# Kernel optimization log

Hardware: AMD Instinct MI355X
Metric: run time of the kernel (lower is better)

The kernel has to match this reference:

```python
import math
import jax, jax.numpy as jnp
import numpy as np

S = 4096          # total packed tokens (b*s with bsz=1)
NUM_HEADS = 16
HEAD_DIM = 80
SCALE = 1.0 / math.sqrt(HEAD_DIM)


def setup_inputs() -> dict:
    key = jax.random.key(0)
    kq, kk, kv = jax.random.split(key, 3)
    q = jax.random.normal(kq, (S, NUM_HEADS, HEAD_DIM), dtype=jnp.float32)
    k = jax.random.normal(kk, (S, NUM_HEADS, HEAD_DIM), dtype=jnp.float32)
    v = jax.random.normal(kv, (S, NUM_HEADS, HEAD_DIM), dtype=jnp.float32)
    # 4 packed sequences of 1024 tokens each (flatten_batch=True, bsz=1)
    cu_seqlens = jnp.array([0, 1024, 2048, 3072, 4096], dtype=jnp.int32)
    return {"q": q, "k": k, "v": v, "bsz": 1, "cu_seqlens": cu_seqlens}


def reference(q, k, v, bsz, cu_seqlens):
    # q/k/v: [(b s), h, d]; flatten_batch=True so bsz == 1
    s = q.shape[0] // bsz
    h, d = q.shape[1], q.shape[2]

    # Block-diagonal mask from cu_seqlens: True inside each packed sequence.
    seg = jnp.searchsorted(cu_seqlens[1:], jnp.arange(s), side="right")  # [s]
    mask = seg[:, None] == seg[None, :]                                  # [s, s]

    # '(b s) h d -> b h s d'
    qb = q.reshape(bsz, s, h, d).transpose(0, 2, 1, 3)
    kb = k.reshape(bsz, s, h, d).transpose(0, 2, 1, 3)
    vb = v.reshape(bsz, s, h, d).transpose(0, 2, 1, 3)

    scores = jnp.einsum("bhsd,bhtd->bhst", qb, kb) * SCALE
    bias = jnp.where(mask, jnp.zeros((), scores.dtype), jnp.finfo(scores.dtype).min)
    attn = jax.nn.softmax((scores + bias).astype(jnp.float32), axis=-1).astype(q.dtype)

    out = jnp.einsum("bhst,bhtd->bhsd", attn, vb)
    # 'b h s d -> (b s) h d'
    return out.transpose(0, 2, 1, 3).reshape(bsz * s, h, d)
```

## Files before the change

kernel.cpp:

```cpp
#include <hip/hip_runtime.h>
#include <hip/hip_bf16.h>
#include <math.h>

#define NTOK 4096
#define NH 16
#define HD 80
#define TOKSTRIDE (NH * HD)
#define QBLK 64
#define KVBLK 64
#define KSTR 88
#define VSTR 72
#define KLBYTES (65 * KSTR * 2)

typedef __bf16 bf16x4 __attribute__((ext_vector_type(4)));
typedef __bf16 bf16x8 __attribute__((ext_vector_type(8)));
typedef float  f32x4  __attribute__((ext_vector_type(4)));
typedef short  short4v __attribute__((ext_vector_type(4)));

#if __has_builtin(__builtin_amdgcn_mfma_f32_16x16x16bf16_1k)
__device__ inline f32x4 mfma16(bf16x4 a, bf16x4 b, f32x4 c) {
  return __builtin_amdgcn_mfma_f32_16x16x16bf16_1k(
      __builtin_bit_cast(short4v, a), __builtin_bit_cast(short4v, b), c, 0, 0, 0);
}
#elif __has_builtin(__builtin_amdgcn_mfma_f32_16x16x16_bf16)
__device__ inline f32x4 mfma16(bf16x4 a, bf16x4 b, f32x4 c) {
  return __builtin_amdgcn_mfma_f32_16x16x16_bf16(a, b, c, 0, 0, 0);
}
#else
__device__ inline f32x4 mfma16(bf16x4 a, bf16x4 b, f32x4 c) {
  asm volatile("v_mfma_f32_16x16x16_bf16 %0, %1, %2, %0"
               : "+v"(c) : "v"(a), "v"(b));
  return c;
}
#endif

__global__ __launch_bounds__(256)
void prepack(const float* __restrict__ kg, const float* __restrict__ vg,
             __bf16* __restrict__ kb, __bf16* __restrict__ vtb) {
  __shared__ __align__(16) __bf16 Vl[HD][72];
  const int tid  = threadIdx.x;
  const int tok0 = blockIdx.x * 64;
  const int h    = blockIdx.y;

  for (int i = tid; i < 64 * 20; i += 256) {
    const int row = i / 20;
    const int c4  = (i % 20) * 4;
    const size_t gsrc = (size_t)(tok0 + row) * TOKSTRIDE + h * HD + c4;
    const size_t gdst = ((size_t)h * NTOK + tok0 + row) * HD + c4;

    float4 fk = *reinterpret_cast<const float4*>(kg + gsrc);
    bf16x4 uk;
    uk[0] = (__bf16)fk.x; uk[1] = (__bf16)fk.y;
    uk[2] = (__bf16)fk.z; uk[3] = (__bf16)fk.w;
    *reinterpret_cast<bf16x4*>(kb + gdst) = uk;

    float4 fv = *reinterpret_cast<const float4*>(vg + gsrc);
    Vl[c4 + 0][row] = (__bf16)fv.x; Vl[c4 + 1][row] = (__bf16)fv.y;
    Vl[c4 + 2][row] = (__bf16)fv.z; Vl[c4 + 3][row] = (__bf16)fv.w;
  }
  __syncthreads();
  for (int i = tid; i < HD * 16; i += 256) {
    const int d = i / 16;
    const int b = i % 16;
    const int pb = ((b & 3) << 2) | (b >> 2);
    bf16x4 val = *reinterpret_cast<const bf16x4*>(&Vl[d][b * 4]);
    *reinterpret_cast<bf16x4*>(vtb + ((size_t)h * HD + d) * NTOK + tok0 + pb * 4) = val;
  }
}

__global__ __launch_bounds__(256, 4)
void vis_attn13(const float* __restrict__ qg, const __bf16* __restrict__ kb,
                const __bf16* __restrict__ vtb, const int* __restrict__ cu,
                int n_cu, float* __restrict__ outg) {
  __shared__ __align__(16) unsigned char smem[22960];
  __bf16* Kl = reinterpret_cast<__bf16*>(smem);
  __bf16* Vt = reinterpret_cast<__bf16*>(smem + KLBYTES);

  const int tid  = threadIdx.x;
  const int w    = tid >> 6;
  const int lane = tid & 63;
  const int lr   = lane & 15;
  const int g    = lane >> 4;

  const int q0 = blockIdx.x * QBLK;
  const int h  = blockIdx.y;

  int kv_start = 0, kv_end = NTOK;
  for (int i = 0; i + 1 < n_cu; ++i) {
    int a = cu[i], b = cu[i + 1];
    if (q0 >= a && q0 < b) { kv_start = a; kv_end = b; }
  }

  for (int i = tid; i < 512 + KSTR; i += 256) {
    if (i < 512) Kl[(i >> 3) * KSTR + 80 + (i & 7)] = (__bf16)0.0f;
    else         Kl[64 * KSTR + (i - 512)]          = (__bf16)0.0f;
  }

  const float qscale = 1.4426950408889634f / sqrtf((float)HD);
  const int qrow = q0 + w * 16 + lr;
  const float* qrp = qg + (size_t)qrow * TOKSTRIDE + h * HD;
  bf16x8 qf[3];
  #pragma unroll
  for (int c = 0; c < 3; ++c) {
    const int dbase = c * 32 + g * 8;
    if (dbase < HD) {
      float4 f0 = *reinterpret_cast<const float4*>(qrp + dbase);
      float4 f1 = *reinterpret_cast<const float4*>(qrp + dbase + 4);
      qf[c][0] = (__bf16)(f0.x * qscale); qf[c][1] = (__bf16)(f0.y * qscale);
      qf[c][2] = (__bf16)(f0.z * qscale); qf[c][3] = (__bf16)(f0.w * qscale);
      qf[c][4] = (__bf16)(f1.x * qscale); qf[c][5] = (__bf16)(f1.y * qscale);
      qf[c][6] = (__bf16)(f1.z * qscale); qf[c][7] = (__bf16)(f1.w * qscale);
    } else {
      #pragma unroll
      for (int j = 0; j < 8; ++j) qf[c][j] = (__bf16)0.0f;
    }
  }

  bf16x4 vfl;
  #pragma unroll
  for (int j = 0; j < 4; ++j) vfl[j] = (lr == 0) ? (__bf16)1.0f : (__bf16)0.0f;

  f32x4 O[6];
  #pragma unroll
  for (int n = 0; n < 6; ++n) O[n] = (f32x4){0.f, 0.f, 0.f, 0.f};

  const __bf16* kbh  = kb  + (size_t)h * NTOK * HD;
  const __bf16* vtbh = vtb + (size_t)h * HD * NTOK;
  const char* gbase = reinterpret_cast<const char*>(kbh);
  const int vdelta = (int)(reinterpret_cast<const char*>(vtbh) - gbase);

  int goff[5], ginc[5], ldsoff[5];
  #pragma unroll
  for (int j = 0; j < 5; ++j) {
    const int c = tid + j * 256;
    if (c < 640) {
      const int row = c / 10, col = (c % 10) * 8;
      goff[j]   = (kv_start * HD + row * HD + col) * 2;
      ginc[j]   = KVBLK * HD * 2;
      ldsoff[j] = (row * KSTR + col) * 2;
    } else {
      const int c2 = c - 640, d = c2 / 8, kc = (c2 % 8) * 8;
      goff[j]   = vdelta + (kv_start + d * NTOK + kc) * 2;
      ginc[j]   = KVBLK * 2;
      ldsoff[j] = KLBYTES + (d * VSTR + kc) * 2;
    }
  }

  bf16x8 st[5];
  #pragma unroll
  for (int j = 0; j < 5; ++j) {
    st[j] = *reinterpret_cast<const bf16x8*>(gbase + goff[j]);
    goff[j] += ginc[j];
  }

  for (int kv0 = kv_start; kv0 < kv_end; kv0 += KVBLK) {
    __syncthreads();
    #pragma unroll
    for (int j = 0; j < 5; ++j)
      *reinterpret_cast<bf16x8*>(smem + ldsoff[j]) = st[j];
    __syncthreads();

    if (kv0 + KVBLK < kv_end) {
      #pragma unroll
      for (int j = 0; j < 5; ++j) {
        st[j] = *reinterpret_cast<const bf16x8*>(gbase + goff[j]);
        goff[j] += ginc[j];
      }
    }

    bf16x4 pf[4];
    __builtin_amdgcn_s_setprio(1);
    #pragma unroll
    for (int t = 0; t < 4; ++t) {
      f32x4 S = (f32x4){0.f, 0.f, 0.f, 0.f};
      #pragma unroll
      for (int c = 0; c < 3; ++c) {
        bf16x8 kf = *reinterpret_cast<const bf16x8*>(&Kl[(t * 16 + lr) * KSTR + c * 32 + g * 8]);
        S = __builtin_amdgcn_mfma_f32_16x16x32_bf16(kf, qf[c], S, 0, 0, 0);
      }
      #pragma unroll
      for (int r = 0; r < 4; ++r)
        pf[t][r] = (__bf16)exp2f(S[r]);
    }
    __builtin_amdgcn_s_setprio(0);

    __builtin_amdgcn_s_setprio(1);
    #pragma unroll
    for (int n = 0; n < 5; ++n) {
      bf16x8 v01 = *reinterpret_cast<const bf16x8*>(&Vt[(n * 16 + lr) * VSTR + g * 16]);
      bf16x8 v23 = *reinterpret_cast<const bf16x8*>(&Vt[(n * 16 + lr) * VSTR + g * 16 + 8]);
      bf16x4 vf0 = __builtin_shufflevector(v01, v01, 0, 1, 2, 3);
      bf16x4 vf1 = __builtin_shufflevector(v01, v01, 4, 5, 6, 7);
      bf16x4 vf2 = __builtin_shufflevector(v23, v23, 0, 1, 2, 3);
      bf16x4 vf3 = __builtin_shufflevector(v23, v23, 4, 5, 6, 7);
      O[n] = mfma16(pf[0], vf0, O[n]);
      O[n] = mfma16(pf[1], vf1, O[n]);
      O[n] = mfma16(pf[2], vf2, O[n]);
      O[n] = mfma16(pf[3], vf3, O[n]);
    }
    #pragma unroll
    for (int t = 0; t < 4; ++t)
      O[5] = mfma16(pf[t], vfl, O[5]);
    __builtin_amdgcn_s_setprio(0);
  }

  float inv[4];
  #pragma unroll
  for (int r = 0; r < 4; ++r) {
    float l = __shfl(O[5][r], lane & 48);
    inv[r] = 1.0f / l;
  }
  const int orow0 = q0 + w * 16 + g * 4;
  #pragma unroll
  for (int n = 0; n < 5; ++n) {
    #pragma unroll
    for (int r = 0; r < 4; ++r)
      outg[(size_t)(orow0 + r) * TOKSTRIDE + h * HD + n * 16 + lr] = O[n][r] * inv[r];
  }
}

__global__ __launch_bounds__(256, 4)
void vis_attn_fb(const float* __restrict__ qg, const float* __restrict__ kg,
                 const float* __restrict__ vg, const int* __restrict__ cu,
                 int n_cu, float* __restrict__ outg) {
  __shared__ __align__(16) __bf16 Kl[KVBLK][104];
  __shared__ __align__(16) __bf16 Vt[HD][72];
  __shared__ __align__(16) __bf16 Pl[64][72];

  const int tid  = threadIdx.x;
  const int w    = tid >> 6;
  const int lane = tid & 63;
  const int lr   = lane & 15;
  const int g    = lane >> 4;
  const int q0 = blockIdx.x * 64;
  const int h  = blockIdx.y;

  int kv_start = 0, kv_end = NTOK;
  for (int i = 0; i + 1 < n_cu; ++i) {
    int a = cu[i], b = cu[i + 1];
    if (q0 >= a && q0 < b) { kv_start = a; kv_end = b; }
  }
  for (int i = tid; i < KVBLK * 16; i += 256)
    Kl[i >> 4][HD + (i & 15)] = (__bf16)0.0f;

  const float qscale = 1.4426950408889634f / sqrtf((float)HD);
  const int qrow = q0 + w * 16 + lr;
  const float* qptr = qg + (size_t)qrow * TOKSTRIDE + h * HD;
  bf16x8 qf[3];
  #pragma unroll
  for (int c = 0; c < 3; ++c) {
    const int dbase = c * 32 + g * 8;
    if (dbase < HD) {
      float4 f0 = *reinterpret_cast<const float4*>(qptr + dbase);
      float4 f1 = *reinterpret_cast<const float4*>(qptr + dbase + 4);
      qf[c][0] = (__bf16)(f0.x * qscale); qf[c][1] = (__bf16)(f0.y * qscale);
      qf[c][2] = (__bf16)(f0.z * qscale); qf[c][3] = (__bf16)(f0.w * qscale);
      qf[c][4] = (__bf16)(f1.x * qscale); qf[c][5] = (__bf16)(f1.y * qscale);
      qf[c][6] = (__bf16)(f1.z * qscale); qf[c][7] = (__bf16)(f1.w * qscale);
    } else {
      #pragma unroll
      for (int j = 0; j < 8; ++j) qf[c][j] = (__bf16)0.0f;
    }
  }

  f32x4 O[5];
  #pragma unroll
  for (int n = 0; n < 5; ++n) O[n] = (f32x4){0.f, 0.f, 0.f, 0.f};
  float m_run[4] = {-1e30f, -1e30f, -1e30f, -1e30f};
  float l_run[4] = {0.f, 0.f, 0.f, 0.f};

  for (int kv0 = kv_start; kv0 < kv_end; kv0 += KVBLK) {
    __syncthreads();
    for (int i = tid; i < KVBLK * (HD / 4); i += 256) {
      const int row = i / (HD / 4);
      const int c4  = (i % (HD / 4)) * 4;
      float4 f = *reinterpret_cast<const float4*>(
          kg + (size_t)(kv0 + row) * TOKSTRIDE + h * HD + c4);
      Kl[row][c4 + 0] = (__bf16)f.x; Kl[row][c4 + 1] = (__bf16)f.y;
      Kl[row][c4 + 2] = (__bf16)f.z; Kl[row][c4 + 3] = (__bf16)f.w;
    }
    for (int i = tid; i < KVBLK * (HD / 4); i += 256) {
      const int row = i / (HD / 4);
      const int c4  = (i % (HD / 4)) * 4;
      float4 f = *reinterpret_cast<const float4*>(
          vg + (size_t)(kv0 + row) * TOKSTRIDE + h * HD + c4);
      Vt[c4 + 0][row] = (__bf16)f.x; Vt[c4 + 1][row] = (__bf16)f.y;
      Vt[c4 + 2][row] = (__bf16)f.z; Vt[c4 + 3][row] = (__bf16)f.w;
    }
    __syncthreads();

    f32x4 S[4];
    #pragma unroll
    for (int t = 0; t < 4; ++t) {
      S[t] = (f32x4){0.f, 0.f, 0.f, 0.f};
      #pragma unroll
      for (int c = 0; c < 3; ++c) {
        bf16x8 kf = *reinterpret_cast<const bf16x8*>(&Kl[t * 16 + lr][c * 32 + g * 8]);
        S[t] = __builtin_amdgcn_mfma_f32_16x16x32_bf16(qf[c], kf, S[t], 0, 0, 0);
      }
    }
    float pmax[4];
    #pragma unroll
    for (int r = 0; r < 4; ++r)
      pmax[r] = fmaxf(fmaxf(S[0][r], S[1][r]), fmaxf(S[2][r], S[3][r]));
    #pragma unroll
    for (int r = 0; r < 4; ++r) {
      pmax[r] = fmaxf(pmax[r], __shfl_xor(pmax[r], 1));
      pmax[r] = fmaxf(pmax[r], __shfl_xor(pmax[r], 2));
      pmax[r] = fmaxf(pmax[r], __shfl_xor(pmax[r], 4));
      pmax[r] = fmaxf(pmax[r], __shfl_xor(pmax[r], 8));
    }
    float alpha[4];
    #pragma unroll
    for (int r = 0; r < 4; ++r) {
      float mn = fmaxf(m_run[r], pmax[r]);
      alpha[r] = exp2f(m_run[r] - mn);
      m_run[r] = mn;
    }
    #pragma unroll
    for (int t = 0; t < 4; ++t) {
      #pragma unroll
      for (int r = 0; r < 4; ++r)
        S[t][r] = exp2f(S[t][r] - m_run[r]);
    }
    float rsum[4];
    #pragma unroll
    for (int r = 0; r < 4; ++r) {
      rsum[r] = (S[0][r] + S[1][r]) + (S[2][r] + S[3][r]);
      rsum[r] += __shfl_xor(rsum[r], 1);
      rsum[r] += __shfl_xor(rsum[r], 2);
      rsum[r] += __shfl_xor(rsum[r], 4);
      rsum[r] += __shfl_xor(rsum[r], 8);
      l_run[r] = l_run[r] * alpha[r] + rsum[r];
    }
    #pragma unroll
    for (int n = 0; n < 5; ++n) {
      #pragma unroll
      for (int r = 0; r < 4; ++r) O[n][r] *= alpha[r];
    }
    #pragma unroll
    for (int t = 0; t < 4; ++t) {
      #pragma unroll
      for (int r = 0; r < 4; ++r)
        Pl[w * 16 + g * 4 + r][t * 16 + lr] = (__bf16)S[t][r];
    }
    #pragma unroll
    for (int kc = 0; kc < 2; ++kc) {
      bf16x8 pf = *reinterpret_cast<const bf16x8*>(&Pl[w * 16 + lr][kc * 32 + g * 8]);
      #pragma unroll
      for (int n = 0; n < 5; ++n) {
        bf16x8 vf = *reinterpret_cast<const bf16x8*>(&Vt[n * 16 + lr][kc * 32 + g * 8]);
        O[n] = __builtin_amdgcn_mfma_f32_16x16x32_bf16(pf, vf, O[n], 0, 0, 0);
      }
    }
  }

  float inv[4];
  #pragma unroll
  for (int r = 0; r < 4; ++r) inv[r] = 1.0f / l_run[r];
  const int orow0 = q0 + w * 16 + g * 4;
  #pragma unroll
  for (int n = 0; n < 5; ++n) {
    #pragma unroll
    for (int r = 0; r < 4; ++r)
      outg[(size_t)(orow0 + r) * TOKSTRIDE + h * HD + n * 16 + lr] = O[n][r] * inv[r];
  }
}

extern "C" void kernel_launch(void* const* d_in, const int* in_sizes, int n_in,
                              void* d_out, int out_size, void* d_ws, size_t ws_size,
                              hipStream_t stream) {
  const float* q  = (const float*)d_in[0];
  const float* k  = (const float*)d_in[1];
  const float* v  = (const float*)d_in[2];
  const int* cu   = (const int*)d_in[4];
  const int n_cu  = in_sizes[4];
  float* out      = (float*)d_out;

  const size_t one = (size_t)NH * NTOK * HD * sizeof(__bf16);

  if (ws_size >= 2 * one) {
    __bf16* kbuf = (__bf16*)d_ws;
    __bf16* vtb  = (__bf16*)((char*)d_ws + one);
    dim3 gp(NTOK / 64, NH);
    prepack<<<gp, 256, 0, stream>>>(k, v, kbuf, vtb);
    dim3 ga(NTOK / QBLK, NH);
    vis_attn13<<<ga, 256, 0, stream>>>(q, kbuf, vtb, cu, n_cu, out);
  } else {
    dim3 gf(NTOK / 64, NH);
    vis_attn_fb<<<gf, 256, 0, stream>>>(q, k, v, cu, n_cu, out);
  }
}
```

Measured before the change: 57.84 us.

## Interleave QK and PV per key tile and overlap head-dim chunk loads

The attention loop now computes exp scores for one 16-key tile and immediately feeds them into the PV MFMAs, instead of materialising all four tiles first. The V transpose in prepack drops its permuted layout for plain contiguous 8-element stores, and the kernel reads V fragments directly per tile. The third QK chunk now reads K columns 48..79 with a Q fragment zeroed for the low half, so the zero-padded K columns and the extra LDS row are no longer needed. This shrinks register pressure and LDS setup, at the cost of an overlapping redundant K read and a different MFMA dependency pattern.

```diff
diff --git a/kernel.cpp b/kernel.cpp
--- a/kernel.cpp
+++ b/kernel.cpp
@@ -10,7 +10,7 @@
 #define KVBLK 64
 #define KSTR 88
 #define VSTR 72
-#define KLBYTES (65 * KSTR * 2)
+#define KLBYTES (64 * KSTR * 2)
 
 typedef __bf16 bf16x4 __attribute__((ext_vector_type(4)));
 typedef __bf16 bf16x8 __attribute__((ext_vector_type(8)));
@@ -59,20 +59,19 @@
     Vl[c4 + 2][row] = (__bf16)fv.z; Vl[c4 + 3][row] = (__bf16)fv.w;
   }
   __syncthreads();
-  for (int i = tid; i < HD * 16; i += 256) {
-    const int d = i / 16;
-    const int b = i % 16;
-    const int pb = ((b & 3) << 2) | (b >> 2);
-    bf16x4 val = *reinterpret_cast<const bf16x4*>(&Vl[d][b * 4]);
-    *reinterpret_cast<bf16x4*>(vtb + ((size_t)h * HD + d) * NTOK + tok0 + pb * 4) = val;
+  for (int i = tid; i < HD * 8; i += 256) {
+    const int d  = i / 8;
+    const int c8 = (i % 8) * 8;
+    bf16x8 val = *reinterpret_cast<const bf16x8*>(&Vl[d][c8]);
+    *reinterpret_cast<bf16x8*>(vtb + ((size_t)h * HD + d) * NTOK + tok0 + c8) = val;
   }
 }
 
 __global__ __launch_bounds__(256, 4)
-void vis_attn13(const float* __restrict__ qg, const __bf16* __restrict__ kb,
+void vis_attn15(const float* __restrict__ qg, const __bf16* __restrict__ kb,
                 const __bf16* __restrict__ vtb, const int* __restrict__ cu,
                 int n_cu, float* __restrict__ outg) {
-  __shared__ __align__(16) unsigned char smem[22960];
+  __shared__ __align__(16) unsigned char smem[22784];
   __bf16* Kl = reinterpret_cast<__bf16*>(smem);
   __bf16* Vt = reinterpret_cast<__bf16*>(smem + KLBYTES);
 
@@ -91,29 +90,32 @@
     if (q0 >= a && q0 < b) { kv_start = a; kv_end = b; }
   }
 
-  for (int i = tid; i < 512 + KSTR; i += 256) {
-    if (i < 512) Kl[(i >> 3) * KSTR + 80 + (i & 7)] = (__bf16)0.0f;
-    else         Kl[64 * KSTR + (i - 512)]          = (__bf16)0.0f;
-  }
-
   const float qscale = 1.4426950408889634f / sqrtf((float)HD);
   const int qrow = q0 + w * 16 + lr;
   const float* qrp = qg + (size_t)qrow * TOKSTRIDE + h * HD;
-  bf16x8 qf[3];
-  #pragma unroll
-  for (int c = 0; c < 3; ++c) {
+  bf16x8 qf[2];
+  #pragma unroll
+  for (int c = 0; c < 2; ++c) {
     const int dbase = c * 32 + g * 8;
-    if (dbase < HD) {
-      float4 f0 = *reinterpret_cast<const float4*>(qrp + dbase);
-      float4 f1 = *reinterpret_cast<const float4*>(qrp + dbase + 4);
-      qf[c][0] = (__bf16)(f0.x * qscale); qf[c][1] = (__bf16)(f0.y * qscale);
-      qf[c][2] = (__bf16)(f0.z * qscale); qf[c][3] = (__bf16)(f0.w * qscale);
-      qf[c][4] = (__bf16)(f1.x * qscale); qf[c][5] = (__bf16)(f1.y * qscale);
-      qf[c][6] = (__bf16)(f1.z * qscale); qf[c][7] = (__bf16)(f1.w * qscale);
-    } else {
-      #pragma unroll
-      for (int j = 0; j < 8; ++j) qf[c][j] = (__bf16)0.0f;
-    }
+    float4 f0 = *reinterpret_cast<const float4*>(qrp + dbase);
+    float4 f1 = *reinterpret_cast<const float4*>(qrp + dbase + 4);
+    qf[c][0] = (__bf16)(f0.x * qscale); qf[c][1] = (__bf16)(f0.y * qscale);
+    qf[c][2] = (__bf16)(f0.z * qscale); qf[c][3] = (__bf16)(f0.w * qscale);
+    qf[c][4] = (__bf16)(f1.x * qscale); qf[c][5] = (__bf16)(f1.y * qscale);
+    qf[c][6] = (__bf16)(f1.z * qscale); qf[c][7] = (__bf16)(f1.w * qscale);
+  }
+  bf16x8 qf2;
+  if (g >= 2) {
+    const int dbase = 48 + g * 8;
+    float4 f0 = *reinterpret_cast<const float4*>(qrp + dbase);
+    float4 f1 = *reinterpret_cast<const float4*>(qrp + dbase + 4);
+    qf2[0] = (__bf16)(f0.x * qscale); qf2[1] = (__bf16)(f0.y * qscale);
+    qf2[2] = (__bf16)(f0.z * qscale); qf2[3] = (__bf16)(f0.w * qscale);
+    qf2[4] = (__bf16)(f1.x * qscale); qf2[5] = (__bf16)(f1.y * qscale);
+    qf2[6] = (__bf16)(f1.z * qscale); qf2[7] = (__bf16)(f1.w * qscale);
+  } else {
+    #pragma unroll
+    for (int j = 0; j < 8; ++j) qf2[j] = (__bf16)0.0f;
   }
 
   bf16x4 vfl;
@@ -168,39 +170,31 @@
       }
     }
 
-    bf16x4 pf[4];
     __builtin_amdgcn_s_setprio(1);
     #pragma unroll
     for (int t = 0; t < 4; ++t) {
+      const int krow = (t * 16 + lr) * KSTR;
       f32x4 S = (f32x4){0.f, 0.f, 0.f, 0.f};
-      #pragma unroll
-      for (int c = 0; c < 3; ++c) {
-        bf16x8 kf = *reinterpret_cast<const bf16x8*>(&Kl[(t * 16 + lr) * KSTR + c * 32 + g * 8]);
-        S = __builtin_amdgcn_mfma_f32_16x16x32_bf16(kf, qf[c], S, 0, 0, 0);
-      }
+      {
+        bf16x8 kf0 = *reinterpret_cast<const bf16x8*>(&Kl[krow + g * 8]);
+        bf16x8 kf1 = *reinterpret_cast<const bf16x8*>(&Kl[krow + 32 + g * 8]);
+        bf16x8 kf2 = *reinterpret_cast<const bf16x8*>(&Kl[krow + 48 + g * 8]);
+        S = __builtin_amdgcn_mfma_f32_16x16x32_bf16(kf0, qf[0], S, 0, 0, 0);
+        S = __builtin_amdgcn_mfma_f32_16x16x32_bf16(kf1, qf[1], S, 0, 0, 0);
+        S = __builtin_amdgcn_mfma_f32_16x16x32_bf16(kf2, qf2, S, 0, 0, 0);
+      }
+      bf16x4 pf;
       #pragma unroll
       for (int r = 0; r < 4; ++r)
-        pf[t][r] = (__bf16)exp2f(S[r]);
-    }
-    __builtin_amdgcn_s_setprio(0);
-
-    __builtin_amdgcn_s_setprio(1);
-    #pragma unroll
-    for (int n = 0; n < 5; ++n) {
-      bf16x8 v01 = *reinterpret_cast<const bf16x8*>(&Vt[(n * 16 + lr) * VSTR + g * 16]);
-      bf16x8 v23 = *reinterpret_cast<const bf16x8*>(&Vt[(n * 16 + lr) * VSTR + g * 16 + 8]);
-      bf16x4 vf0 = __builtin_shufflevector(v01, v01, 0, 1, 2, 3);
-      bf16x4 vf1 = __builtin_shufflevector(v01, v01, 4, 5, 6, 7);
-      bf16x4 vf2 = __builtin_shufflevector(v23, v23, 0, 1, 2, 3);
-      bf16x4 vf3 = __builtin_shufflevector(v23, v23, 4, 5, 6, 7);
-      O[n] = mfma16(pf[0], vf0, O[n]);
-      O[n] = mfma16(pf[1], vf1, O[n]);
-      O[n] = mfma16(pf[2], vf2, O[n]);
-      O[n] = mfma16(pf[3], vf3, O[n]);
-    }
-    #pragma unroll
-    for (int t = 0; t < 4; ++t)
-      O[5] = mfma16(pf[t], vfl, O[5]);
+        pf[r] = (__bf16)exp2f(S[r]);
+
+      #pragma unroll
+      for (int n = 0; n < 5; ++n) {
+        bf16x4 vf = *reinterpret_cast<const bf16x4*>(&Vt[(n * 16 + lr) * VSTR + t * 16 + g * 4]);
+        O[n] = mfma16(pf, vf, O[n]);
+      }
+      O[5] = mfma16(pf, vfl, O[5]);
+    }
     __builtin_amdgcn_s_setprio(0);
   }
 
@@ -385,7 +379,7 @@
     dim3 gp(NTOK / 64, NH);
     prepack<<<gp, 256, 0, stream>>>(k, v, kbuf, vtb);
     dim3 ga(NTOK / QBLK, NH);
-    vis_attn13<<<ga, 256, 0, stream>>>(q, kbuf, vtb, cu, n_cu, out);
+    vis_attn15<<<ga, 256, 0, stream>>>(q, kbuf, vtb, cu, n_cu, out);
   } else {
     dim3 gf(NTOK / 64, NH);
     vis_attn_fb<<<gf, 256, 0, stream>>>(q, k, v, cu, n_cu, out);
```

New measurement: 62.81 us. +8.6%, slower.
